# Kernel tuning notes

Hardware: AMD Instinct MI355X
Metric: run time of the kernel (lower is better)

Reference implementation:

```python
import jax, jax.numpy as jnp
import numpy as np

T, B, D, H = 128, 128, 1024, 1024

def setup_inputs() -> dict:
    key = jax.random.key(0)
    ks = jax.random.split(key, 3)
    x = jax.random.normal(ks[0], (T, B, D), jnp.float32)
    reset = (jax.random.uniform(ks[1], (T, B)) < 0.05).astype(jnp.float32)
    h0 = jnp.zeros((1, B, H), jnp.float32)
    c0 = jnp.zeros((1, B, H), jnp.float32)
    W = jax.random.normal(ks[2], (D + H, 4 * H), jnp.float32) / np.float32(np.sqrt(D + H))
    b = jnp.zeros((4 * H,), jnp.float32)
    return {"x": x, "h0": h0, "c0": c0, "reset": reset, "W": W, "b": b}

def _lstm_scan(x, h0, c0, reset, W, b):
    Hh = h0.shape[-1]
    def step(carry, inp):
        h, c = carry
        x_t, r_t = inp
        m = (1.0 - r_t)[:, None]           # reset wipes state
        h = h * m
        c = c * m
        gated = jnp.concatenate([x_t, h], axis=-1) @ W + b  # [B, 4H]
        i, g, f, o = jnp.split(gated, 4, axis=-1)
        f = jax.nn.sigmoid(f + 1.0)        # forget-gate bias of +1 as in source
        c = f * c + jax.nn.sigmoid(i) * jnp.tanh(g)
        h = jax.nn.sigmoid(o) * jnp.tanh(c)
        return (h, c), h
    (hT, cT), ys = jax.lax.scan(step, (h0[0], c0[0]), (x, reset))
    # torch.cat(outputs, dim=0) on per-step [B,H] slices -> [T*B, H]
    out = ys.reshape(-1, Hh)
    return out, hT, cT

def reference(x, h0, c0, reset, W, b):
    out, hT, cT = _lstm_scan(x, h0, c0, reset, W, b)
    return out, hT[None], cT[None]
```

## Files before the change

kernel.cpp:

```cpp
#include <hip/hip_runtime.h>
#include <math.h>

#define T_STEPS 128
#define B_SZ 128
#define D_SZ 1024
#define H_SZ 1024
#define G4 4096
#define KW 2048

typedef __attribute__((ext_vector_type(8))) short bf16x8;
typedef __attribute__((ext_vector_type(4))) float f32x4;
typedef unsigned short ushort_t;
typedef unsigned int uint_t;
typedef unsigned long long ull_t;

__device__ __forceinline__ float sigf(float x) { return 1.0f / (1.0f + __expf(-x)); }
__device__ __forceinline__ float tanhfast(float x) { return 1.0f - 2.0f * sigf(-2.0f * x); }

__device__ __forceinline__ ushort_t f2bf(float f) {
  uint_t u = __float_as_uint(f);
  return (ushort_t)((u + 0x7fffu + ((u >> 16) & 1u)) >> 16);
}
__device__ __forceinline__ float bf2f(ushort_t s) {
  return __uint_as_float(((uint_t)s) << 16);
}

#define GLOAD_LDS16(gp, lp)                                                  \
  __builtin_amdgcn_global_load_lds(                                          \
      (const __attribute__((address_space(1))) unsigned int*)(const void*)(gp), \
      (__attribute__((address_space(3))) unsigned int*)(void*)(lp), 16, 0, 0)

__global__ __launch_bounds__(256) void convert_x(const float* __restrict__ x,
                                                 ushort_t* __restrict__ xbf) {
  const size_t i8 = ((size_t)blockIdx.x * 256 + threadIdx.x) * 8;
  if (i8 + 8 > (size_t)T_STEPS * B_SZ * D_SZ) return;
  float4 a = *(const float4*)&x[i8];
  float4 b = *(const float4*)&x[i8 + 4];
  ushort_t o[8] = {f2bf(a.x), f2bf(a.y), f2bf(a.z), f2bf(a.w),
                   f2bf(b.x), f2bf(b.y), f2bf(b.z), f2bf(b.w)};
  *(uint4*)&xbf[i8] = *(uint4*)o;
}

__global__ __launch_bounds__(256) void transpose_w(const float* __restrict__ W,
                                                   ushort_t* __restrict__ WT) {
  __shared__ float t[32][33];
  const int tx = threadIdx.x & 31;
  const int ty = threadIdx.x >> 5;
  const int k0 = blockIdx.x * 32;
  const int n0 = blockIdx.y * 32;
#pragma unroll
  for (int i = 0; i < 4; ++i)
    t[ty + i * 8][tx] = W[(size_t)(k0 + ty + i * 8) * G4 + n0 + tx];
  __syncthreads();
#pragma unroll
  for (int i = 0; i < 4; ++i)
    WT[(size_t)(n0 + ty + i * 8) * KW + k0 + tx] = f2bf(t[tx][ty + i * 8]);
}

__global__ __launch_bounds__(256) void init_state(const float* __restrict__ h0,
                                                  const float* __restrict__ reset0,
                                                  ushort_t* __restrict__ hbf0) {
  const int i = blockIdx.x * 256 + threadIdx.x;
  if (i >= B_SZ * H_SZ) return;
  hbf0[i] = f2bf(h0[i] * (1.0f - reset0[i >> 10]));
}

__global__ __launch_bounds__(256) void xw_mfma3(const ushort_t* __restrict__ xbf,
                                                const ushort_t* __restrict__ WT,
                                                const float* __restrict__ bias,
                                                ushort_t* __restrict__ xwg) {
  __shared__ ushort_t Asb[2][128 * 64];
  __shared__ ushort_t Bsb[2][128 * 64];

  const int bid = blockIdx.x;
  const int xcd = bid & 7;
  const int ib = bid >> 3;
  const int mt = (ib >> 5) * 8 + (ib & 7);
  const int nt = xcd * 4 + ((ib >> 3) & 3);
  const int m0 = mt * 128, n0 = nt * 128;
  const int tid = threadIdx.x, lane = tid & 63, wid = tid >> 6;
  const int wr = wid >> 1, wc = wid & 1;
  const int lr = lane & 15, ko = lane >> 4;
  const int srow = lane >> 3;
  const int skb = (lane & 7) * 16;

  f32x4 acc[4][4] = {};

#define XW_STAGE(buf, kt)                                                      \
  {                                                                            \
    const int k0b = (kt) * 128;                                                \
    _Pragma("unroll") for (int i = 0; i < 4; ++i) {                            \
      const int c = wid * 4 + i;                                               \
      const int row = c * 8 + srow;                                            \
      const int sw = skb ^ ((row & 7) << 4);                                   \
      GLOAD_LDS16((const char*)xbf + (size_t)(m0 + row) * 2048 + k0b + sw,     \
                  (char*)&Asb[buf][0] + c * 1024);                             \
      GLOAD_LDS16((const char*)WT + (size_t)(n0 + row) * 4096 + k0b + sw,      \
                  (char*)&Bsb[buf][0] + c * 1024);                             \
    }                                                                          \
  }

  XW_STAGE(0, 0);
  __syncthreads();
  const int xsw = (lr & 7) << 4;
  for (int kt = 0; kt < 16; ++kt) {
    if (kt + 1 < 16) XW_STAGE((kt + 1) & 1, kt + 1);
    const char* Ab = (const char*)&Asb[kt & 1][0] + (wr * 64 + lr) * 128;
    const char* Bb = (const char*)&Bsb[kt & 1][0] + (wc * 64 + lr) * 128;
#pragma unroll
    for (int ks = 0; ks < 2; ++ks) {
      const int kb = (ks * 64 + ko * 16) ^ xsw;
      bf16x8 a[4], b[4];
#pragma unroll
      for (int mi = 0; mi < 4; ++mi) a[mi] = *(const bf16x8*)(Ab + mi * 2048 + kb);
#pragma unroll
      for (int ni = 0; ni < 4; ++ni) b[ni] = *(const bf16x8*)(Bb + ni * 2048 + kb);
#pragma unroll
      for (int mi = 0; mi < 4; ++mi)
#pragma unroll
        for (int ni = 0; ni < 4; ++ni)
          acc[mi][ni] = __builtin_amdgcn_mfma_f32_16x16x32_bf16(a[mi], b[ni], acc[mi][ni], 0, 0, 0);
    }
    __syncthreads();
  }

  const int rr = ko * 4;
#pragma unroll
  for (int ni = 0; ni < 4; ++ni) {
    const int n = n0 + wc * 64 + ni * 16 + lr;
    const int g = n >> 10;
    const int jtn = (n & 1023) >> 4;
    const float bn = bias[n];
#pragma unroll
    for (int mi = 0; mi < 4; ++mi) {
      const int m = m0 + wr * 64 + mi * 16 + rr;
      const int tt = m >> 7;
      const int btp = (m & 127) >> 5;
      const int r32 = m & 31;
      ushort_t tmp[4];
#pragma unroll
      for (int r = 0; r < 4; ++r) tmp[r] = f2bf(acc[mi][ni][r] + bn);
      *(ull_t*)(xwg + (((size_t)tt * 4 + btp) * 64 + jtn) * 2048 + g * 512 + lr * 32 + r32) =
          *(ull_t*)tmp;
    }
  }
}

__global__ __launch_bounds__(512) void lstm_persist6(
    const ushort_t* __restrict__ hbf0,
    const float* __restrict__ c0,
    const float* __restrict__ reset,
    const ushort_t* __restrict__ xwg,
    const ushort_t* __restrict__ WT,
    float* __restrict__ out,
    ushort_t* __restrict__ hring,
    uint_t* __restrict__ bar)
{
  __shared__ ushort_t WhL[64 * 512];
  __shared__ ushort_t Ah[32 * 1024];
  __shared__ float sc[2][4][16][17];

  const int tid = threadIdx.x;
  const int bid = blockIdx.x;
  const int jt = bid & 63;
  const int btp = bid >> 6;
  const int b0 = btp * 32;
  const int lane = tid & 63;
  const int wid = tid >> 6;
  const int g = wid & 3;
  const int mh = wid >> 2;
  const int lr = lane & 15;
  const int ko = lane >> 4;
  const size_t SE = (size_t)B_SZ * H_SZ;

  uint_t* const arr = bar + btp * 256;

  for (int p = 0; p < 8; ++p) {
    const int id = p * 512 + tid;
    const int wrw = id >> 6;
    const int kb = (id & 63) * 16;
    const int n = (wrw >> 4) * H_SZ + jt * 16 + (wrw & 15);
    const uint4 v = *(const uint4*)((const char*)WT + (size_t)n * 4096 + 2048 + kb);
    *(uint4*)((char*)WhL + wrw * 1024 + (kb ^ ((wrw & 7) << 4))) = v;
  }

  const char* wrow = (const char*)WT + (size_t)(g * H_SZ + jt * 16 + lr) * 4096;
  bf16x8 breg[16];
#pragma unroll
  for (int q = 0; q < 16; ++q)
    breg[q] = *(const bf16x8*)(wrow + 3072 + q * 64 + ko * 16);

  const int row = tid >> 4;
  const int col = tid & 15;
  const int b = b0 + row;
  const int j = jt * 16 + col;
  const size_t so = (size_t)b * H_SZ + j;
  float creg = c0[so] * (1.0f - reset[b]);

  const int swzl = (lr & 7) << 4;
  const char* aBase = (const char*)Ah + (mh * 16 + lr) * 2048;
  const char* bBase = (const char*)WhL + (g * 16 + lr) * 1024;

  ushort_t xq0, xq1, xq2, xq3;
  {
    const ushort_t* xp = xwg + (((size_t)btp) * 64 + jt) * 2048 + col * 32 + row;
    xq0 = xp[0]; xq1 = xp[512]; xq2 = xp[1024]; xq3 = xp[1536];
  }
  float mn = 1.0f - reset[B_SZ + b];

  for (int t = 0; t < T_STEPS; ++t) {
    if (t > 0) {
      uint_t it = 0;
      for (;;) {
        const uint_t v = __hip_atomic_load(&arr[lane], __ATOMIC_RELAXED,
                                           __HIP_MEMORY_SCOPE_AGENT);
        if (__all((int)v >= t)) break;
        __builtin_amdgcn_s_sleep(1);
        if (++it > 1000000u) break;
      }
    }
    const char* hsrc = (t == 0) ? (const char*)hbf0
                                : (const char*)(hring + (size_t)t * SE);
#pragma unroll
    for (int i = 0; i < 8; ++i) {
      const int c = wid * 8 + i;
      const int hrow = c >> 1;
      const int half = (c & 1) * 1024;
      const int kb = half + lane * 16;
      const int src = kb ^ ((hrow & 7) << 4);
      GLOAD_LDS16(hsrc + (size_t)(b0 + hrow) * 2048 + src,
                  (char*)Ah + hrow * 2048 + half);
    }
    __syncthreads();

    f32x4 ac0 = {}, ac1 = {}, ac2 = {}, ac3 = {};
#pragma unroll
    for (int q = 0; q < 4; ++q) {
      bf16x8 a0 = *(const bf16x8*)(aBase + (((q * 4 + 0) * 64 + ko * 16) ^ swzl));
      bf16x8 b0f = *(const bf16x8*)(bBase + (((q * 4 + 0) * 64 + ko * 16) ^ swzl));
      ac0 = __builtin_amdgcn_mfma_f32_16x16x32_bf16(a0, b0f, ac0, 0, 0, 0);
      bf16x8 a1 = *(const bf16x8*)(aBase + (((q * 4 + 1) * 64 + ko * 16) ^ swzl));
      bf16x8 b1f = *(const bf16x8*)(bBase + (((q * 4 + 1) * 64 + ko * 16) ^ swzl));
      ac1 = __builtin_amdgcn_mfma_f32_16x16x32_bf16(a1, b1f, ac1, 0, 0, 0);
      bf16x8 a2 = *(const bf16x8*)(aBase + (((q * 4 + 2) * 64 + ko * 16) ^ swzl));
      bf16x8 b2f = *(const bf16x8*)(bBase + (((q * 4 + 2) * 64 + ko * 16) ^ swzl));
      ac2 = __builtin_amdgcn_mfma_f32_16x16x32_bf16(a2, b2f, ac2, 0, 0, 0);
      bf16x8 a3 = *(const bf16x8*)(aBase + (((q * 4 + 3) * 64 + ko * 16) ^ swzl));
      bf16x8 b3f = *(const bf16x8*)(bBase + (((q * 4 + 3) * 64 + ko * 16) ^ swzl));
      ac3 = __builtin_amdgcn_mfma_f32_16x16x32_bf16(a3, b3f, ac3, 0, 0, 0);
    }
#pragma unroll
    for (int q = 0; q < 4; ++q) {
      bf16x8 a0 = *(const bf16x8*)(aBase + (((16 + q * 4 + 0) * 64 + ko * 16) ^ swzl));
      ac0 = __builtin_amdgcn_mfma_f32_16x16x32_bf16(a0, breg[q * 4 + 0], ac0, 0, 0, 0);
      bf16x8 a1 = *(const bf16x8*)(aBase + (((16 + q * 4 + 1) * 64 + ko * 16) ^ swzl));
      ac1 = __builtin_amdgcn_mfma_f32_16x16x32_bf16(a1, breg[q * 4 + 1], ac1, 0, 0, 0);
      bf16x8 a2 = *(const bf16x8*)(aBase + (((16 + q * 4 + 2) * 64 + ko * 16) ^ swzl));
      ac2 = __builtin_amdgcn_mfma_f32_16x16x32_bf16(a2, breg[q * 4 + 2], ac2, 0, 0, 0);
      bf16x8 a3 = *(const bf16x8*)(aBase + (((16 + q * 4 + 3) * 64 + ko * 16) ^ swzl));
      ac3 = __builtin_amdgcn_mfma_f32_16x16x32_bf16(a3, breg[q * 4 + 3], ac3, 0, 0, 0);
    }
    const f32x4 acc = (ac0 + ac1) + (ac2 + ac3);
#pragma unroll
    for (int r = 0; r < 4; ++r) sc[mh][g][ko * 4 + r][lr] = acc[r];
    __syncthreads();

    const float gi = sc[row >> 4][0][row & 15][col] + bf2f(xq0);
    const float gg = sc[row >> 4][1][row & 15][col] + bf2f(xq1);
    const float gf = sc[row >> 4][2][row & 15][col] + bf2f(xq2);
    const float go = sc[row >> 4][3][row & 15][col] + bf2f(xq3);
    const float f = sigf(gf + 1.0f);
    const float cn = f * creg + sigf(gi) * tanhfast(gg);
    const float hn = sigf(go) * tanhfast(cn);
    out[(size_t)t * SE + so] = hn;
    creg = cn * mn;

    if (t < T_STEPS - 1) {
      const uint_t hm = (uint_t)f2bf(hn * mn);
      const uint_t h1 = (uint_t)__shfl_down((int)hm, 1);
      const uint_t h2 = (uint_t)__shfl_down((int)hm, 2);
      const uint_t h3 = (uint_t)__shfl_down((int)hm, 3);
      if ((col & 3) == 0) {
        const ull_t pk = (ull_t)(hm & 0xffffu) | ((ull_t)(h1 & 0xffffu) << 16) |
                         ((ull_t)(h2 & 0xffffu) << 32) | ((ull_t)(h3 & 0xffffu) << 48);
        __hip_atomic_store((ull_t*)(hring + (size_t)(t + 1) * SE + so), pk,
                           __ATOMIC_RELAXED, __HIP_MEMORY_SCOPE_AGENT);
      }
      asm volatile("s_waitcnt vmcnt(0)" ::: "memory");
      __syncthreads();

      if (tid == 0)
        __hip_atomic_store(&arr[jt], (uint_t)(t + 1),
                           __ATOMIC_RELAXED, __HIP_MEMORY_SCOPE_AGENT);

      const ushort_t* xp = xwg + (((size_t)(t + 1) * 4 + btp) * 64 + jt) * 2048 + col * 32 + row;
      xq0 = xp[0]; xq1 = xp[512]; xq2 = xp[1024]; xq3 = xp[1536];
      mn = (t + 1 < T_STEPS - 1) ? (1.0f - reset[(size_t)(t + 2) * B_SZ + b]) : 1.0f;
    } else {
      float* hT = out + (size_t)T_STEPS * SE;
      float* cT = hT + SE;
      hT[so] = hn;
      cT[so] = cn;
    }
  }
}

extern "C" void kernel_launch(void* const* d_in, const int* in_sizes, int n_in,
                              void* d_out, int out_size, void* d_ws, size_t ws_size,
                              hipStream_t stream) {
  (void)in_sizes; (void)n_in; (void)out_size; (void)ws_size;
  const float* x = (const float*)d_in[0];
  const float* h0 = (const float*)d_in[1];
  const float* c0 = (const float*)d_in[2];
  const float* reset = (const float*)d_in[3];
  const float* W = (const float*)d_in[4];
  const float* bias = (const float*)d_in[5];
  float* out = (float*)d_out;

  const size_t TB = (size_t)T_STEPS * B_SZ;
  const size_t SE = (size_t)B_SZ * H_SZ;

  char* p = (char*)d_ws;
  uint_t* bar = (uint_t*)p;               p += 4096;
  ushort_t* WT = (ushort_t*)p;            p += (size_t)G4 * KW * 2;
  ushort_t* xbf = (ushort_t*)p;           p += TB * D_SZ * 2;
  ushort_t* xwg = (ushort_t*)p;           p += TB * G4 * 2;
  ushort_t* hbf0 = (ushort_t*)p;          p += SE * 2;
  ushort_t* hring = (ushort_t*)p;         p += (size_t)T_STEPS * SE * 2;

  hipMemsetAsync(bar, 0, 4096, stream);
  convert_x<<<dim3((int)(TB * D_SZ / 8 / 256)), 256, 0, stream>>>(x, xbf);
  transpose_w<<<dim3(KW / 32, G4 / 32), 256, 0, stream>>>(W, WT);
  init_state<<<dim3((int)((SE + 255) / 256)), 256, 0, stream>>>(h0, reset, hbf0);
  xw_mfma3<<<dim3(4096), 256, 0, stream>>>(xbf, WT, bias, xwg);

  lstm_persist6<<<dim3(256), 512, 0, stream>>>(hbf0, c0, reset, xwg, WT, out, hring, bar);
}
```

Baseline: 768.9 us.

## Ping-pong two independent batch groups per block to hide recurrent-step latency

Each persistent block now owns two independent 16-row batch groups instead of one 32-row group. It alternates between them: while one group's GEMM and gate math run, the other group's h-state loads and barrier poll are in flight. The K dimension is split across wave halves, and partial sums are added in LDS. The intent is to hide the inter-block sync and global h reload latency of the sequential scan behind compute. In exchange it adds more __syncthreads per step and twice as many barrier counters, and each GEMM runs on half the batch rows.

```diff
diff --git a/kernel.cpp b/kernel.cpp
--- a/kernel.cpp
+++ b/kernel.cpp
@@ -146,7 +146,7 @@
   }
 }
 
-__global__ __launch_bounds__(512) void lstm_persist6(
+__global__ __launch_bounds__(512) void lstm_pp(
     const ushort_t* __restrict__ hbf0,
     const float* __restrict__ c0,
     const float* __restrict__ reset,
@@ -157,150 +157,226 @@
     uint_t* __restrict__ bar)
 {
   __shared__ ushort_t WhL[64 * 512];
-  __shared__ ushort_t Ah[32 * 1024];
+  __shared__ ushort_t Ah0[16 * 1024];
+  __shared__ ushort_t Ah1[16 * 1024];
   __shared__ float sc[2][4][16][17];
 
   const int tid = threadIdx.x;
   const int bid = blockIdx.x;
   const int jt = bid & 63;
-  const int btp = bid >> 6;
-  const int b0 = btp * 32;
+  const int p = bid >> 6;
+  const int b0 = p * 16;
+  const int b1 = (p + 4) * 16;
   const int lane = tid & 63;
   const int wid = tid >> 6;
-  const int g = wid & 3;
-  const int mh = wid >> 2;
+  const int gw = wid & 3;
+  const int kh = wid >> 2;
   const int lr = lane & 15;
   const int ko = lane >> 4;
   const size_t SE = (size_t)B_SZ * H_SZ;
 
-  uint_t* const arr = bar + btp * 256;
-
-  for (int p = 0; p < 8; ++p) {
-    const int id = p * 512 + tid;
+  uint_t* const arr0 = bar + p * 256;
+  uint_t* const arr1 = bar + (p + 4) * 256;
+
+  for (int q = 0; q < 8; ++q) {
+    const int id = q * 512 + tid;
     const int wrw = id >> 6;
     const int kb = (id & 63) * 16;
     const int n = (wrw >> 4) * H_SZ + jt * 16 + (wrw & 15);
     const uint4 v = *(const uint4*)((const char*)WT + (size_t)n * 4096 + 2048 + kb);
     *(uint4*)((char*)WhL + wrw * 1024 + (kb ^ ((wrw & 7) << 4))) = v;
   }
-
-  const char* wrow = (const char*)WT + (size_t)(g * H_SZ + jt * 16 + lr) * 4096;
+  const char* wrow = (const char*)WT + (size_t)(gw * H_SZ + jt * 16 + lr) * 4096;
   bf16x8 breg[16];
 #pragma unroll
   for (int q = 0; q < 16; ++q)
     breg[q] = *(const bf16x8*)(wrow + 3072 + q * 64 + ko * 16);
 
-  const int row = tid >> 4;
-  const int col = tid & 15;
-  const int b = b0 + row;
-  const int j = jt * 16 + col;
-  const size_t so = (size_t)b * H_SZ + j;
-  float creg = c0[so] * (1.0f - reset[b]);
-
-  const int swzl = (lr & 7) << 4;
-  const char* aBase = (const char*)Ah + (mh * 16 + lr) * 2048;
-  const char* bBase = (const char*)WhL + (g * 16 + lr) * 1024;
-
+  const int et = tid & 255;
+  const int erow = et >> 4;
+  const int ecol = et & 15;
+  const int eb = ((tid >> 8) ? b1 : b0) + erow;
+  const int ej = jt * 16 + ecol;
+  const size_t eso = (size_t)eb * H_SZ + ej;
+  float creg = c0[eso] * (1.0f - reset[eb]);
+  const int ebtp = eb >> 5, er32 = eb & 31;
   ushort_t xq0, xq1, xq2, xq3;
   {
-    const ushort_t* xp = xwg + (((size_t)btp) * 64 + jt) * 2048 + col * 32 + row;
+    const ushort_t* xp = xwg + ((size_t)ebtp * 64 + jt) * 2048 + ecol * 32 + er32;
     xq0 = xp[0]; xq1 = xp[512]; xq2 = xp[1024]; xq3 = xp[1536];
   }
-  float mn = 1.0f - reset[B_SZ + b];
-
-  for (int t = 0; t < T_STEPS; ++t) {
-    if (t > 0) {
-      uint_t it = 0;
-      for (;;) {
-        const uint_t v = __hip_atomic_load(&arr[lane], __ATOMIC_RELAXED,
-                                           __HIP_MEMORY_SCOPE_AGENT);
-        if (__all((int)v >= t)) break;
-        __builtin_amdgcn_s_sleep(1);
-        if (++it > 1000000u) break;
-      }
-    }
-    const char* hsrc = (t == 0) ? (const char*)hbf0
-                                : (const char*)(hring + (size_t)t * SE);
+  float mn = 1.0f - reset[B_SZ + eb];
+
+  const int swzl = (lr & 7) << 4;
+  const char* a0B = (const char*)Ah0 + lr * 2048;
+  const char* a1B = (const char*)Ah1 + lr * 2048;
+  const char* bB = (const char*)WhL + (gw * 16 + lr) * 1024;
+  const int kbase = kh * 1024;
+
+  if (wid < 4) {
 #pragma unroll
     for (int i = 0; i < 8; ++i) {
       const int c = wid * 8 + i;
-      const int hrow = c >> 1;
-      const int half = (c & 1) * 1024;
-      const int kb = half + lane * 16;
-      const int src = kb ^ ((hrow & 7) << 4);
-      GLOAD_LDS16(hsrc + (size_t)(b0 + hrow) * 2048 + src,
-                  (char*)Ah + hrow * 2048 + half);
-    }
-    __syncthreads();
-
-    f32x4 ac0 = {}, ac1 = {}, ac2 = {}, ac3 = {};
-#pragma unroll
-    for (int q = 0; q < 4; ++q) {
-      bf16x8 a0 = *(const bf16x8*)(aBase + (((q * 4 + 0) * 64 + ko * 16) ^ swzl));
-      bf16x8 b0f = *(const bf16x8*)(bBase + (((q * 4 + 0) * 64 + ko * 16) ^ swzl));
-      ac0 = __builtin_amdgcn_mfma_f32_16x16x32_bf16(a0, b0f, ac0, 0, 0, 0);
-      bf16x8 a1 = *(const bf16x8*)(aBase + (((q * 4 + 1) * 64 + ko * 16) ^ swzl));
-      bf16x8 b1f = *(const bf16x8*)(bBase + (((q * 4 + 1) * 64 + ko * 16) ^ swzl));
-      ac1 = __builtin_amdgcn_mfma_f32_16x16x32_bf16(a1, b1f, ac1, 0, 0, 0);
-      bf16x8 a2 = *(const bf16x8*)(aBase + (((q * 4 + 2) * 64 + ko * 16) ^ swzl));
-      bf16x8 b2f = *(const bf16x8*)(bBase + (((q * 4 + 2) * 64 + ko * 16) ^ swzl));
-      ac2 = __builtin_amdgcn_mfma_f32_16x16x32_bf16(a2, b2f, ac2, 0, 0, 0);
-      bf16x8 a3 = *(const bf16x8*)(aBase + (((q * 4 + 3) * 64 + ko * 16) ^ swzl));
-      bf16x8 b3f = *(const bf16x8*)(bBase + (((q * 4 + 3) * 64 + ko * 16) ^ swzl));
-      ac3 = __builtin_amdgcn_mfma_f32_16x16x32_bf16(a3, b3f, ac3, 0, 0, 0);
-    }
-#pragma unroll
-    for (int q = 0; q < 4; ++q) {
-      bf16x8 a0 = *(const bf16x8*)(aBase + (((16 + q * 4 + 0) * 64 + ko * 16) ^ swzl));
-      ac0 = __builtin_amdgcn_mfma_f32_16x16x32_bf16(a0, breg[q * 4 + 0], ac0, 0, 0, 0);
-      bf16x8 a1 = *(const bf16x8*)(aBase + (((16 + q * 4 + 1) * 64 + ko * 16) ^ swzl));
-      ac1 = __builtin_amdgcn_mfma_f32_16x16x32_bf16(a1, breg[q * 4 + 1], ac1, 0, 0, 0);
-      bf16x8 a2 = *(const bf16x8*)(aBase + (((16 + q * 4 + 2) * 64 + ko * 16) ^ swzl));
-      ac2 = __builtin_amdgcn_mfma_f32_16x16x32_bf16(a2, breg[q * 4 + 2], ac2, 0, 0, 0);
-      bf16x8 a3 = *(const bf16x8*)(aBase + (((16 + q * 4 + 3) * 64 + ko * 16) ^ swzl));
-      ac3 = __builtin_amdgcn_mfma_f32_16x16x32_bf16(a3, breg[q * 4 + 3], ac3, 0, 0, 0);
-    }
-    const f32x4 acc = (ac0 + ac1) + (ac2 + ac3);
-#pragma unroll
-    for (int r = 0; r < 4; ++r) sc[mh][g][ko * 4 + r][lr] = acc[r];
-    __syncthreads();
-
-    const float gi = sc[row >> 4][0][row & 15][col] + bf2f(xq0);
-    const float gg = sc[row >> 4][1][row & 15][col] + bf2f(xq1);
-    const float gf = sc[row >> 4][2][row & 15][col] + bf2f(xq2);
-    const float go = sc[row >> 4][3][row & 15][col] + bf2f(xq3);
-    const float f = sigf(gf + 1.0f);
-    const float cn = f * creg + sigf(gi) * tanhfast(gg);
-    const float hn = sigf(go) * tanhfast(cn);
-    out[(size_t)t * SE + so] = hn;
-    creg = cn * mn;
-
-    if (t < T_STEPS - 1) {
-      const uint_t hm = (uint_t)f2bf(hn * mn);
-      const uint_t h1 = (uint_t)__shfl_down((int)hm, 1);
-      const uint_t h2 = (uint_t)__shfl_down((int)hm, 2);
-      const uint_t h3 = (uint_t)__shfl_down((int)hm, 3);
-      if ((col & 3) == 0) {
-        const ull_t pk = (ull_t)(hm & 0xffffu) | ((ull_t)(h1 & 0xffffu) << 16) |
-                         ((ull_t)(h2 & 0xffffu) << 32) | ((ull_t)(h3 & 0xffffu) << 48);
-        __hip_atomic_store((ull_t*)(hring + (size_t)(t + 1) * SE + so), pk,
-                           __ATOMIC_RELAXED, __HIP_MEMORY_SCOPE_AGENT);
+      const int row = c >> 1;
+      const int hk = (c & 1) * 1024;
+      const int kb = hk + lane * 16;
+      const int src = kb ^ ((row & 7) << 4);
+      GLOAD_LDS16((const char*)hbf0 + (size_t)(b0 + row) * 2048 + src,
+                  (char*)Ah0 + row * 2048 + hk);
+    }
+  }
+
+#define PP_GEMM(AB, ACC)                                                       \
+  {                                                                            \
+    _Pragma("unroll") for (int ks = 0; ks < 16; ++ks) {                        \
+      const int kb = ks * 64 + ko * 16;                                        \
+      bf16x8 a = *(const bf16x8*)((AB) + ((kbase + kb) ^ swzl));               \
+      bf16x8 bb = kh ? breg[ks] : *(const bf16x8*)(bB + (kb ^ swzl));          \
+      ACC = __builtin_amdgcn_mfma_f32_16x16x32_bf16(a, bb, ACC, 0, 0, 0);      \
+    }                                                                          \
+  }
+
+#define PP_POLL(ARR, TGT)                                                      \
+  {                                                                            \
+    uint_t it = 0;                                                             \
+    for (;;) {                                                                 \
+      const uint_t v = __hip_atomic_load(&(ARR)[lane], __ATOMIC_RELAXED,       \
+                                         __HIP_MEMORY_SCOPE_AGENT);            \
+      if (__all((int)v >= (int)(TGT))) break;                                  \
+      __builtin_amdgcn_s_sleep(1);                                             \
+      if (++it > 1000000u) break;                                              \
+    }                                                                          \
+  }
+
+  float* const hT = out + (size_t)T_STEPS * SE;
+  float* const cT = hT + SE;
+
+  for (int t = 0; t < T_STEPS; ++t) {
+    if (wid < 4) asm volatile("s_waitcnt vmcnt(0)" ::: "memory");
+    __syncthreads();
+    f32x4 acc = {};
+    PP_GEMM(a0B, acc);
+    if (t > 0 && wid == 0) PP_POLL(arr1, t);
+#pragma unroll
+    for (int r = 0; r < 4; ++r) sc[kh][gw][ko * 4 + r][lr] = acc[r];
+    __syncthreads();
+    if (wid >= 4) {
+      const char* hs = (t == 0) ? (const char*)hbf0
+                                : (const char*)(hring + (size_t)t * SE);
+#pragma unroll
+      for (int i = 0; i < 8; ++i) {
+        const int c = (wid - 4) * 8 + i;
+        const int row = c >> 1;
+        const int hk = (c & 1) * 1024;
+        const int kb = hk + lane * 16;
+        const int src = kb ^ ((row & 7) << 4);
+        GLOAD_LDS16(hs + (size_t)(b1 + row) * 2048 + src,
+                    (char*)Ah1 + row * 2048 + hk);
+      }
+    }
+    float hn0 = 0.0f;
+    if (tid < 256) {
+      const float gi = sc[0][0][erow][ecol] + sc[1][0][erow][ecol] + bf2f(xq0);
+      const float gg = sc[0][1][erow][ecol] + sc[1][1][erow][ecol] + bf2f(xq1);
+      const float gf = sc[0][2][erow][ecol] + sc[1][2][erow][ecol] + bf2f(xq2);
+      const float go = sc[0][3][erow][ecol] + sc[1][3][erow][ecol] + bf2f(xq3);
+      const float f = sigf(gf + 1.0f);
+      const float cn = f * creg + sigf(gi) * tanhfast(gg);
+      const float hn = sigf(go) * tanhfast(cn);
+      creg = cn * mn;
+      hn0 = hn;
+      if (t < T_STEPS - 1) {
+        const uint_t hm = (uint_t)f2bf(hn * mn);
+        const uint_t h1 = (uint_t)__shfl_down((int)hm, 1);
+        const uint_t h2 = (uint_t)__shfl_down((int)hm, 2);
+        const uint_t h3 = (uint_t)__shfl_down((int)hm, 3);
+        if ((ecol & 3) == 0) {
+          const ull_t pk = (ull_t)(hm & 0xffffu) | ((ull_t)(h1 & 0xffffu) << 16) |
+                           ((ull_t)(h2 & 0xffffu) << 32) | ((ull_t)(h3 & 0xffffu) << 48);
+          __hip_atomic_store((ull_t*)(hring + (size_t)(t + 1) * SE + eso), pk,
+                             __ATOMIC_RELAXED, __HIP_MEMORY_SCOPE_AGENT);
+        }
+      } else {
+        hT[eso] = hn;
+        cT[eso] = cn;
       }
       asm volatile("s_waitcnt vmcnt(0)" ::: "memory");
-      __syncthreads();
-
-      if (tid == 0)
-        __hip_atomic_store(&arr[jt], (uint_t)(t + 1),
-                           __ATOMIC_RELAXED, __HIP_MEMORY_SCOPE_AGENT);
-
-      const ushort_t* xp = xwg + (((size_t)(t + 1) * 4 + btp) * 64 + jt) * 2048 + col * 32 + row;
-      xq0 = xp[0]; xq1 = xp[512]; xq2 = xp[1024]; xq3 = xp[1536];
-      mn = (t + 1 < T_STEPS - 1) ? (1.0f - reset[(size_t)(t + 2) * B_SZ + b]) : 1.0f;
-    } else {
-      float* hT = out + (size_t)T_STEPS * SE;
-      float* cT = hT + SE;
-      hT[so] = hn;
-      cT[so] = cn;
+    }
+    __syncthreads();
+    if (tid == 0 && t < T_STEPS - 1)
+      __hip_atomic_store(&arr0[jt], (uint_t)(t + 1), __ATOMIC_RELAXED,
+                         __HIP_MEMORY_SCOPE_AGENT);
+    if (tid < 256) {
+      out[(size_t)t * SE + eso] = hn0;
+      if (t < T_STEPS - 1) {
+        const ushort_t* xp =
+            xwg + (((size_t)(t + 1) * 4 + ebtp) * 64 + jt) * 2048 + ecol * 32 + er32;
+        xq0 = xp[0]; xq1 = xp[512]; xq2 = xp[1024]; xq3 = xp[1536];
+        mn = (t + 1 < T_STEPS - 1) ? (1.0f - reset[(size_t)(t + 2) * B_SZ + eb]) : 1.0f;
+      }
+    }
+    if (wid >= 4) asm volatile("s_waitcnt vmcnt(0)" ::: "memory");
+    __syncthreads();
+
+    f32x4 acc2 = {};
+    PP_GEMM(a1B, acc2);
+    if (t < T_STEPS - 1 && wid == 0) PP_POLL(arr0, t + 1);
+#pragma unroll
+    for (int r = 0; r < 4; ++r) sc[kh][gw][ko * 4 + r][lr] = acc2[r];
+    __syncthreads();
+    if (wid < 4 && t < T_STEPS - 1) {
+      const char* hs = (const char*)(hring + (size_t)(t + 1) * SE);
+#pragma unroll
+      for (int i = 0; i < 8; ++i) {
+        const int c = wid * 8 + i;
+        const int row = c >> 1;
+        const int hk = (c & 1) * 1024;
+        const int kb = hk + lane * 16;
+        const int src = kb ^ ((row & 7) << 4);
+        GLOAD_LDS16(hs + (size_t)(b0 + row) * 2048 + src,
+                    (char*)Ah0 + row * 2048 + hk);
+      }
+    }
+    float hn1 = 0.0f;
+    if (tid >= 256) {
+      const float gi = sc[0][0][erow][ecol] + sc[1][0][erow][ecol] + bf2f(xq0);
+      const float gg = sc[0][1][erow][ecol] + sc[1][1][erow][ecol] + bf2f(xq1);
+      const float gf = sc[0][2][erow][ecol] + sc[1][2][erow][ecol] + bf2f(xq2);
+      const float go = sc[0][3][erow][ecol] + sc[1][3][erow][ecol] + bf2f(xq3);
+      const float f = sigf(gf + 1.0f);
+      const float cn = f * creg + sigf(gi) * tanhfast(gg);
+      const float hn = sigf(go) * tanhfast(cn);
+      creg = cn * mn;
+      hn1 = hn;
+      if (t < T_STEPS - 1) {
+        const uint_t hm = (uint_t)f2bf(hn * mn);
+        const uint_t h1 = (uint_t)__shfl_down((int)hm, 1);
+        const uint_t h2 = (uint_t)__shfl_down((int)hm, 2);
+        const uint_t h3 = (uint_t)__shfl_down((int)hm, 3);
+        if ((ecol & 3) == 0) {
+          const ull_t pk = (ull_t)(hm & 0xffffu) | ((ull_t)(h1 & 0xffffu) << 16) |
+                           ((ull_t)(h2 & 0xffffu) << 32) | ((ull_t)(h3 & 0xffffu) << 48);
+          __hip_atomic_store((ull_t*)(hring + (size_t)(t + 1) * SE + eso), pk,
+                             __ATOMIC_RELAXED, __HIP_MEMORY_SCOPE_AGENT);
+        }
+      } else {
+        hT[eso] = hn;
+        cT[eso] = cn;
+      }
+      asm volatile("s_waitcnt vmcnt(0)" ::: "memory");
+    }
+    __syncthreads();
+    if (tid == 256 && t < T_STEPS - 1)
+      __hip_atomic_store(&arr1[jt], (uint_t)(t + 1), __ATOMIC_RELAXED,
+                         __HIP_MEMORY_SCOPE_AGENT);
+    if (tid >= 256) {
+      out[(size_t)t * SE + eso] = hn1;
+      if (t < T_STEPS - 1) {
+        const ushort_t* xp =
+            xwg + (((size_t)(t + 1) * 4 + ebtp) * 64 + jt) * 2048 + ecol * 32 + er32;
+        xq0 = xp[0]; xq1 = xp[512]; xq2 = xp[1024]; xq3 = xp[1536];
+        mn = (t + 1 < T_STEPS - 1) ? (1.0f - reset[(size_t)(t + 2) * B_SZ + eb]) : 1.0f;
+      }
     }
   }
 }
@@ -321,18 +397,18 @@
   const size_t SE = (size_t)B_SZ * H_SZ;
 
   char* p = (char*)d_ws;
-  uint_t* bar = (uint_t*)p;               p += 4096;
+  uint_t* bar = (uint_t*)p;               p += 16384;
   ushort_t* WT = (ushort_t*)p;            p += (size_t)G4 * KW * 2;
   ushort_t* xbf = (ushort_t*)p;           p += TB * D_SZ * 2;
   ushort_t* xwg = (ushort_t*)p;           p += TB * G4 * 2;
   ushort_t* hbf0 = (ushort_t*)p;          p += SE * 2;
   ushort_t* hring = (ushort_t*)p;         p += (size_t)T_STEPS * SE * 2;
 
-  hipMemsetAsync(bar, 0, 4096, stream);
+  hipMemsetAsync(bar, 0, 16384, stream);
   convert_x<<<dim3((int)(TB * D_SZ / 8 / 256)), 256, 0, stream>>>(x, xbf);
   transpose_w<<<dim3(KW / 32, G4 / 32), 256, 0, stream>>>(W, WT);
   init_state<<<dim3((int)((SE + 255) / 256)), 256, 0, stream>>>(h0, reset, hbf0);
   xw_mfma3<<<dim3(4096), 256, 0, stream>>>(xbf, WT, bias, xwg);
 
-  lstm_persist6<<<dim3(256), 512, 0, stream>>>(hbf0, c0, reset, xwg, WT, out, hring, bar);
-}
+  lstm_pp<<<dim3(256), 512, 0, stream>>>(hbf0, c0, reset, xwg, WT, out, hring, bar);
+}
```

Result: slower. 889.8 us (+15.7%).

## Fuse input projection GEMM into persistent LSTM kernel, computed per step off critical path

Applied to the files above, without the earlier changes.

Removes the separate x·W_x GEMM kernel and its bf16 gate buffer. The persistent recurrent kernel now stages the next timestep's x rows into shared memory and computes each block's slice of the input projection right after signalling its barrier, overlapping it with the wait for other blocks. The barrier spin is also restricted to one wavefront followed by a block sync. The trade-off is that W_x fragments are read from global memory every step and more MFMA work lands inside the serial loop. If the hidden latency is shorter than that work, each step gets longer.

```diff
diff --git a/kernel.cpp b/kernel.cpp
--- a/kernel.cpp
+++ b/kernel.cpp
@@ -65,93 +65,13 @@
   hbf0[i] = f2bf(h0[i] * (1.0f - reset0[i >> 10]));
 }
 
-__global__ __launch_bounds__(256) void xw_mfma3(const ushort_t* __restrict__ xbf,
-                                                const ushort_t* __restrict__ WT,
-                                                const float* __restrict__ bias,
-                                                ushort_t* __restrict__ xwg) {
-  __shared__ ushort_t Asb[2][128 * 64];
-  __shared__ ushort_t Bsb[2][128 * 64];
-
-  const int bid = blockIdx.x;
-  const int xcd = bid & 7;
-  const int ib = bid >> 3;
-  const int mt = (ib >> 5) * 8 + (ib & 7);
-  const int nt = xcd * 4 + ((ib >> 3) & 3);
-  const int m0 = mt * 128, n0 = nt * 128;
-  const int tid = threadIdx.x, lane = tid & 63, wid = tid >> 6;
-  const int wr = wid >> 1, wc = wid & 1;
-  const int lr = lane & 15, ko = lane >> 4;
-  const int srow = lane >> 3;
-  const int skb = (lane & 7) * 16;
-
-  f32x4 acc[4][4] = {};
-
-#define XW_STAGE(buf, kt)                                                      \
-  {                                                                            \
-    const int k0b = (kt) * 128;                                                \
-    _Pragma("unroll") for (int i = 0; i < 4; ++i) {                            \
-      const int c = wid * 4 + i;                                               \
-      const int row = c * 8 + srow;                                            \
-      const int sw = skb ^ ((row & 7) << 4);                                   \
-      GLOAD_LDS16((const char*)xbf + (size_t)(m0 + row) * 2048 + k0b + sw,     \
-                  (char*)&Asb[buf][0] + c * 1024);                             \
-      GLOAD_LDS16((const char*)WT + (size_t)(n0 + row) * 4096 + k0b + sw,      \
-                  (char*)&Bsb[buf][0] + c * 1024);                             \
-    }                                                                          \
-  }
-
-  XW_STAGE(0, 0);
-  __syncthreads();
-  const int xsw = (lr & 7) << 4;
-  for (int kt = 0; kt < 16; ++kt) {
-    if (kt + 1 < 16) XW_STAGE((kt + 1) & 1, kt + 1);
-    const char* Ab = (const char*)&Asb[kt & 1][0] + (wr * 64 + lr) * 128;
-    const char* Bb = (const char*)&Bsb[kt & 1][0] + (wc * 64 + lr) * 128;
-#pragma unroll
-    for (int ks = 0; ks < 2; ++ks) {
-      const int kb = (ks * 64 + ko * 16) ^ xsw;
-      bf16x8 a[4], b[4];
-#pragma unroll
-      for (int mi = 0; mi < 4; ++mi) a[mi] = *(const bf16x8*)(Ab + mi * 2048 + kb);
-#pragma unroll
-      for (int ni = 0; ni < 4; ++ni) b[ni] = *(const bf16x8*)(Bb + ni * 2048 + kb);
-#pragma unroll
-      for (int mi = 0; mi < 4; ++mi)
-#pragma unroll
-        for (int ni = 0; ni < 4; ++ni)
-          acc[mi][ni] = __builtin_amdgcn_mfma_f32_16x16x32_bf16(a[mi], b[ni], acc[mi][ni], 0, 0, 0);
-    }
-    __syncthreads();
-  }
-
-  const int rr = ko * 4;
-#pragma unroll
-  for (int ni = 0; ni < 4; ++ni) {
-    const int n = n0 + wc * 64 + ni * 16 + lr;
-    const int g = n >> 10;
-    const int jtn = (n & 1023) >> 4;
-    const float bn = bias[n];
-#pragma unroll
-    for (int mi = 0; mi < 4; ++mi) {
-      const int m = m0 + wr * 64 + mi * 16 + rr;
-      const int tt = m >> 7;
-      const int btp = (m & 127) >> 5;
-      const int r32 = m & 31;
-      ushort_t tmp[4];
-#pragma unroll
-      for (int r = 0; r < 4; ++r) tmp[r] = f2bf(acc[mi][ni][r] + bn);
-      *(ull_t*)(xwg + (((size_t)tt * 4 + btp) * 64 + jtn) * 2048 + g * 512 + lr * 32 + r32) =
-          *(ull_t*)tmp;
-    }
-  }
-}
-
-__global__ __launch_bounds__(512) void lstm_persist6(
+__global__ __launch_bounds__(512) void lstm_persist8(
     const ushort_t* __restrict__ hbf0,
     const float* __restrict__ c0,
     const float* __restrict__ reset,
-    const ushort_t* __restrict__ xwg,
+    const ushort_t* __restrict__ xbf,
     const ushort_t* __restrict__ WT,
+    const float* __restrict__ bias,
     float* __restrict__ out,
     ushort_t* __restrict__ hring,
     uint_t* __restrict__ bar)
@@ -159,6 +79,7 @@
   __shared__ ushort_t WhL[64 * 512];
   __shared__ ushort_t Ah[32 * 1024];
   __shared__ float sc[2][4][16][17];
+  __shared__ ushort_t xwL[4][32][16];
 
   const int tid = threadIdx.x;
   const int bid = blockIdx.x;
@@ -167,7 +88,7 @@
   const int b0 = btp * 32;
   const int lane = tid & 63;
   const int wid = tid >> 6;
-  const int g = wid & 3;
+  const int gw = wid & 3;
   const int mh = wid >> 2;
   const int lr = lane & 15;
   const int ko = lane >> 4;
@@ -175,20 +96,22 @@
 
   uint_t* const arr = bar + btp * 256;
 
-  for (int p = 0; p < 8; ++p) {
-    const int id = p * 512 + tid;
+  for (int q = 0; q < 8; ++q) {
+    const int id = q * 512 + tid;
     const int wrw = id >> 6;
     const int kb = (id & 63) * 16;
     const int n = (wrw >> 4) * H_SZ + jt * 16 + (wrw & 15);
     const uint4 v = *(const uint4*)((const char*)WT + (size_t)n * 4096 + 2048 + kb);
     *(uint4*)((char*)WhL + wrw * 1024 + (kb ^ ((wrw & 7) << 4))) = v;
   }
-
-  const char* wrow = (const char*)WT + (size_t)(g * H_SZ + jt * 16 + lr) * 4096;
+  const char* wrow = (const char*)WT + (size_t)(gw * H_SZ + jt * 16 + lr) * 4096;
   bf16x8 breg[16];
 #pragma unroll
   for (int q = 0; q < 16; ++q)
     breg[q] = *(const bf16x8*)(wrow + 3072 + q * 64 + ko * 16);
+
+  const float bias_n = bias[gw * H_SZ + jt * 16 + lr];
+  const f32x4 bias4 = {bias_n, bias_n, bias_n, bias_n};
 
   const int row = tid >> 4;
   const int col = tid & 15;
@@ -196,41 +119,62 @@
   const int j = jt * 16 + col;
   const size_t so = (size_t)b * H_SZ + j;
   float creg = c0[so] * (1.0f - reset[b]);
+  float mn = 1.0f - reset[B_SZ + b];
 
   const int swzl = (lr & 7) << 4;
   const char* aBase = (const char*)Ah + (mh * 16 + lr) * 2048;
-  const char* bBase = (const char*)WhL + (g * 16 + lr) * 1024;
-
-  ushort_t xq0, xq1, xq2, xq3;
-  {
-    const ushort_t* xp = xwg + (((size_t)btp) * 64 + jt) * 2048 + col * 32 + row;
-    xq0 = xp[0]; xq1 = xp[512]; xq2 = xp[1024]; xq3 = xp[1536];
-  }
-  float mn = 1.0f - reset[B_SZ + b];
+  const char* bBase = (const char*)WhL + (gw * 16 + lr) * 1024;
+  const char* xbB = (const char*)WT + (size_t)(gw * H_SZ + jt * 16 + lr) * 4096;
+
+#define STAGE_A(SRCB)                                                          \
+  {                                                                            \
+    _Pragma("unroll") for (int i = 0; i < 8; ++i) {                            \
+      const int cc = wid * 8 + i;                                              \
+      const int ar = cc >> 1;                                                  \
+      const int hf = (cc & 1) * 1024;                                          \
+      const int kb = hf + lane * 16;                                           \
+      GLOAD_LDS16((SRCB) + (size_t)ar * 2048 + (kb ^ ((ar & 7) << 4)),         \
+                  (char*)Ah + ar * 2048 + hf);                                 \
+    }                                                                          \
+  }
+
+#define XGEMM_TO_XWL()                                                         \
+  {                                                                            \
+    f32x4 xacc = bias4;                                                        \
+    _Pragma("unroll") for (int ks = 0; ks < 32; ++ks) {                        \
+      bf16x8 a = *(const bf16x8*)(aBase + ((ks * 64 + ko * 16) ^ swzl));       \
+      bf16x8 bx = *(const bf16x8*)(xbB + ks * 64 + ko * 16);                   \
+      xacc = __builtin_amdgcn_mfma_f32_16x16x32_bf16(a, bx, xacc, 0, 0, 0);    \
+    }                                                                          \
+    _Pragma("unroll") for (int r = 0; r < 4; ++r)                              \
+        xwL[gw][mh * 16 + ko * 4 + r][lr] = f2bf(xacc[r]);                     \
+  }
+
+  STAGE_A((const char*)xbf + (size_t)b0 * 2048);
+  __syncthreads();
+  XGEMM_TO_XWL();
+  __syncthreads();
+
+  float* const hT = out + (size_t)T_STEPS * SE;
+  float* const cT = hT + SE;
 
   for (int t = 0; t < T_STEPS; ++t) {
     if (t > 0) {
-      uint_t it = 0;
-      for (;;) {
-        const uint_t v = __hip_atomic_load(&arr[lane], __ATOMIC_RELAXED,
-                                           __HIP_MEMORY_SCOPE_AGENT);
-        if (__all((int)v >= t)) break;
-        __builtin_amdgcn_s_sleep(1);
-        if (++it > 1000000u) break;
+      if (wid == 0) {
+        uint_t it = 0;
+        for (;;) {
+          const uint_t v = __hip_atomic_load(&arr[lane], __ATOMIC_RELAXED,
+                                             __HIP_MEMORY_SCOPE_AGENT);
+          if (__all((int)v >= t)) break;
+          __builtin_amdgcn_s_sleep(1);
+          if (++it > 1000000u) break;
+        }
       }
-    }
-    const char* hsrc = (t == 0) ? (const char*)hbf0
-                                : (const char*)(hring + (size_t)t * SE);
-#pragma unroll
-    for (int i = 0; i < 8; ++i) {
-      const int c = wid * 8 + i;
-      const int hrow = c >> 1;
-      const int half = (c & 1) * 1024;
-      const int kb = half + lane * 16;
-      const int src = kb ^ ((hrow & 7) << 4);
-      GLOAD_LDS16(hsrc + (size_t)(b0 + hrow) * 2048 + src,
-                  (char*)Ah + hrow * 2048 + half);
-    }
+      __syncthreads();
+    }
+    const char* hb = (t == 0) ? (const char*)hbf0
+                              : (const char*)(hring + (size_t)t * SE);
+    STAGE_A(hb + (size_t)b0 * 2048);
     __syncthreads();
 
     f32x4 ac0 = {}, ac1 = {}, ac2 = {}, ac3 = {};
@@ -262,17 +206,19 @@
     }
     const f32x4 acc = (ac0 + ac1) + (ac2 + ac3);
 #pragma unroll
-    for (int r = 0; r < 4; ++r) sc[mh][g][ko * 4 + r][lr] = acc[r];
+    for (int r = 0; r < 4; ++r) sc[mh][gw][ko * 4 + r][lr] = acc[r];
     __syncthreads();
 
-    const float gi = sc[row >> 4][0][row & 15][col] + bf2f(xq0);
-    const float gg = sc[row >> 4][1][row & 15][col] + bf2f(xq1);
-    const float gf = sc[row >> 4][2][row & 15][col] + bf2f(xq2);
-    const float go = sc[row >> 4][3][row & 15][col] + bf2f(xq3);
+    if (t + 1 < T_STEPS)
+      STAGE_A((const char*)xbf + ((size_t)(t + 1) * B_SZ + b0) * 2048);
+
+    const float gi = sc[row >> 4][0][row & 15][col] + bf2f(xwL[0][row][col]);
+    const float gg = sc[row >> 4][1][row & 15][col] + bf2f(xwL[1][row][col]);
+    const float gf = sc[row >> 4][2][row & 15][col] + bf2f(xwL[2][row][col]);
+    const float go = sc[row >> 4][3][row & 15][col] + bf2f(xwL[3][row][col]);
     const float f = sigf(gf + 1.0f);
     const float cn = f * creg + sigf(gi) * tanhfast(gg);
     const float hn = sigf(go) * tanhfast(cn);
-    out[(size_t)t * SE + so] = hn;
     creg = cn * mn;
 
     if (t < T_STEPS - 1) {
@@ -286,21 +232,21 @@
         __hip_atomic_store((ull_t*)(hring + (size_t)(t + 1) * SE + so), pk,
                            __ATOMIC_RELAXED, __HIP_MEMORY_SCOPE_AGENT);
       }
-      asm volatile("s_waitcnt vmcnt(0)" ::: "memory");
-      __syncthreads();
-
-      if (tid == 0)
-        __hip_atomic_store(&arr[jt], (uint_t)(t + 1),
-                           __ATOMIC_RELAXED, __HIP_MEMORY_SCOPE_AGENT);
-
-      const ushort_t* xp = xwg + (((size_t)(t + 1) * 4 + btp) * 64 + jt) * 2048 + col * 32 + row;
-      xq0 = xp[0]; xq1 = xp[512]; xq2 = xp[1024]; xq3 = xp[1536];
-      mn = (t + 1 < T_STEPS - 1) ? (1.0f - reset[(size_t)(t + 2) * B_SZ + b]) : 1.0f;
     } else {
-      float* hT = out + (size_t)T_STEPS * SE;
-      float* cT = hT + SE;
       hT[so] = hn;
       cT[so] = cn;
+    }
+    asm volatile("s_waitcnt vmcnt(0)" ::: "memory");
+    __syncthreads();
+
+    if (tid == 0 && t < T_STEPS - 1)
+      __hip_atomic_store(&arr[jt], (uint_t)(t + 1), __ATOMIC_RELAXED,
+                         __HIP_MEMORY_SCOPE_AGENT);
+    out[(size_t)t * SE + so] = hn;
+
+    if (t < T_STEPS - 1) {
+      mn = (t + 1 < T_STEPS - 1) ? (1.0f - reset[(size_t)(t + 2) * B_SZ + b]) : 1.0f;
+      XGEMM_TO_XWL();
     }
   }
 }
@@ -321,18 +267,17 @@
   const size_t SE = (size_t)B_SZ * H_SZ;
 
   char* p = (char*)d_ws;
-  uint_t* bar = (uint_t*)p;               p += 4096;
+  uint_t* bar = (uint_t*)p;               p += 16384;
   ushort_t* WT = (ushort_t*)p;            p += (size_t)G4 * KW * 2;
   ushort_t* xbf = (ushort_t*)p;           p += TB * D_SZ * 2;
-  ushort_t* xwg = (ushort_t*)p;           p += TB * G4 * 2;
   ushort_t* hbf0 = (ushort_t*)p;          p += SE * 2;
   ushort_t* hring = (ushort_t*)p;         p += (size_t)T_STEPS * SE * 2;
 
-  hipMemsetAsync(bar, 0, 4096, stream);
+  hipMemsetAsync(bar, 0, 16384, stream);
   convert_x<<<dim3((int)(TB * D_SZ / 8 / 256)), 256, 0, stream>>>(x, xbf);
   transpose_w<<<dim3(KW / 32, G4 / 32), 256, 0, stream>>>(W, WT);
   init_state<<<dim3((int)((SE + 255) / 256)), 256, 0, stream>>>(h0, reset, hbf0);
-  xw_mfma3<<<dim3(4096), 256, 0, stream>>>(xbf, WT, bias, xwg);
-
-  lstm_persist6<<<dim3(256), 512, 0, stream>>>(hbf0, c0, reset, xwg, WT, out, hring, bar);
-}
+
+  lstm_persist8<<<dim3(256), 512, 0, stream>>>(hbf0, c0, reset, xbf, WT, bias,
+                                               out, hring, bar);
+}
```

Result: slower. 1.461 ms (+90.0%).
